# Performance work log

Measured on AMD Instinct MI355X. Metric: run time of the kernel, lower is better.

Reference implementation:

```python
import jax, jax.numpy as jnp
import numpy as np

D_MODEL = 2048
D_FFN = 8192
RANK = 16
MOD_SCALE = 0.1
EPS = 1e-6


def setup_inputs() -> dict:
    key = jax.random.key(0)
    ks = jax.random.split(key, 8)
    B, S = 2, 2048
    init_scale = 0.01
    return {
        'hidden_states': jax.random.normal(ks[0], (B, S, D_MODEL), jnp.float32),
        'attn_output': jax.random.normal(ks[1], (B, S, D_MODEL), jnp.float32),
        'A': jax.random.normal(ks[2], (D_MODEL, RANK), jnp.float32) * (init_scale / np.sqrt(D_MODEL)),
        'Bmat': jax.random.normal(ks[3], (RANK, D_FFN), jnp.float32) * (init_scale / np.sqrt(RANK)),
        'W_in': jax.random.normal(ks[4], (D_FFN, D_MODEL), jnp.float32) * 0.02,  # gate_proj.weight
        'W_up': jax.random.normal(ks[5], (D_FFN, D_MODEL), jnp.float32) * 0.02,  # up_proj.weight
        'W_down': jax.random.normal(ks[6], (D_MODEL, D_FFN), jnp.float32) * 0.02,  # down_proj.weight
        'gamma': jnp.ones((D_MODEL,), jnp.float32),  # post_attention_layernorm (RMSNorm) weight
    }


def _rmsnorm(x, gamma):
    var = jnp.mean(x * x, axis=-1, keepdims=True)
    return x * jax.lax.rsqrt(var + EPS) * gamma


def reference(hidden_states, attn_output, A, Bmat, W_in, W_up, W_down, gamma):
    residual = hidden_states
    # Neuro-plastic modulation: [B,S,r]
    modulation = MOD_SCALE * jnp.tanh(jnp.einsum('bsd,dr->bsr', attn_output, A))
    # NPT applies post-attn norm to the residual (not residual+attn)
    h = _rmsnorm(residual, gamma)  # [B,S,d_model]
    # Fused per-token weight delta: delta_w^T @ h == B^T ((A^T h) * mod)
    hA = jnp.einsum('bsd,dr->bsr', h, A)  # [B,S,r]
    delta_out = jnp.einsum('bsr,rf->bsf', hA * modulation, Bmat)  # [B,S,d_ffn]
    gate = jax.nn.silu(jnp.einsum('bsd,fd->bsf', h, W_in) + delta_out)
    up = jnp.einsum('bsd,fd->bsf', h, W_up)
    out = jnp.einsum('bsf,df->bsd', gate * up, W_down)
    return residual + out
```

## Files before the change

### kernel.cpp

```cpp
#include <hip/hip_runtime.h>
#include <cstdint>
#include <cstddef>

#define D_MODEL 2048
#define D_FFN   8192
#define RANK    16
#define EPS     1e-6f
#define MOD_SCALE 0.1f

typedef float    f32x4 __attribute__((ext_vector_type(4)));
typedef _Float16 half8 __attribute__((ext_vector_type(8)));

__device__ __forceinline__ void async_load16(const void* g, void* l) {
  __builtin_amdgcn_global_load_lds(
      (const __attribute__((address_space(1))) uint32_t*)g,
      (__attribute__((address_space(3))) uint32_t*)l,
      16, 0, 0);
}

__device__ __forceinline__ void stage_round(const _Float16* __restrict__ g,
                                            size_t stride, _Float16* l, int tid) {
  const int row = tid >> 3;
  const int cs  = (tid & 7) ^ (row & 7);
  async_load16(g + (size_t)row * stride + (size_t)cs * 8, l + tid * 8);
}

__device__ __forceinline__ half8 frag64(const _Float16* base, int row, int ck) {
  return *(const half8*)&base[row * 64 + ((ck ^ (row & 7)) * 8)];
}

#define BAR()   __builtin_amdgcn_s_barrier()
#define PRIO1() __builtin_amdgcn_s_setprio(1)
#define PRIO0() __builtin_amdgcn_s_setprio(0)
#define VMW(n)  asm volatile("s_waitcnt vmcnt(" #n ")" ::: "memory")

__global__ __launch_bounds__(256) void convert3_f32_f16(
    const float* __restrict__ s0, const float* __restrict__ s1,
    const float* __restrict__ s2,
    _Float16* __restrict__ d0, _Float16* __restrict__ d1,
    _Float16* __restrict__ d2)
{
  const int w = blockIdx.x >> 13;
  const float*   s = (w == 0) ? s0 : (w == 1) ? s1 : s2;
  _Float16*      d = (w == 0) ? d0 : (w == 1) ? d1 : d2;
  size_t i = ((size_t)(blockIdx.x & 8191) * 256 + threadIdx.x) * 8;
  f32x4 a = *(const f32x4*)(s + i);
  f32x4 b = *(const f32x4*)(s + i + 4);
  half8 h;
  #pragma unroll
  for (int j = 0; j < 4; ++j) { h[j] = (_Float16)a[j]; h[4+j] = (_Float16)b[j]; }
  *(half8*)(d + i) = h;
}

__global__ __launch_bounds__(256) void convert_f32_f16(
    const float* __restrict__ s, _Float16* __restrict__ d)
{
  size_t i = ((size_t)blockIdx.x * 256 + threadIdx.x) * 8;
  f32x4 a = *(const f32x4*)(s + i);
  f32x4 b = *(const f32x4*)(s + i + 4);
  half8 h;
  #pragma unroll
  for (int j = 0; j < 4; ++j) { h[j] = (_Float16)a[j]; h[4+j] = (_Float16)b[j]; }
  *(half8*)(d + i) = h;
}

__global__ __launch_bounds__(256) void prep_kernel(
    const float* __restrict__ hs, const float* __restrict__ attn,
    const float* __restrict__ Amat, const float* __restrict__ gamma,
    _Float16* __restrict__ h16, float* __restrict__ cmat)
{
  const int token = blockIdx.x;
  const int tid   = threadIdx.x;
  const int lane  = tid & 63;
  const int wv    = tid >> 6;
  const size_t tb = (size_t)token * D_MODEL;
  const int base  = tid * 8;

  f32x4 x0 = *(const f32x4*)(hs + tb + base);
  f32x4 x1 = *(const f32x4*)(hs + tb + base + 4);
  f32x4 a0 = *(const f32x4*)(attn + tb + base);
  f32x4 a1 = *(const f32x4*)(attn + tb + base + 4);

  float ss = 0.f;
  #pragma unroll
  for (int j = 0; j < 4; ++j) ss += x0[j]*x0[j] + x1[j]*x1[j];
  #pragma unroll
  for (int off = 32; off > 0; off >>= 1) ss += __shfl_xor(ss, off, 64);

  __shared__ float red[4];
  __shared__ float redp[4][RANK];
  __shared__ float redh[4][RANK];
  if (lane == 0) red[wv] = ss;
  __syncthreads();
  const float tot = red[0] + red[1] + red[2] + red[3];
  const float rms = rsqrtf(tot * (1.0f / D_MODEL) + EPS);

  f32x4 g0 = *(const f32x4*)(gamma + base);
  f32x4 g1 = *(const f32x4*)(gamma + base + 4);
  float hv[8], av[8];
  #pragma unroll
  for (int j = 0; j < 4; ++j) {
    hv[j]   = x0[j] * rms * g0[j];
    hv[4+j] = x1[j] * rms * g1[j];
    av[j]   = a0[j];
    av[4+j] = a1[j];
  }
  half8 hh;
  #pragma unroll
  for (int j = 0; j < 8; ++j) hh[j] = (_Float16)hv[j];
  *(half8*)(h16 + tb + base) = hh;

  float pa[RANK], ph[RANK];
  #pragma unroll
  for (int r = 0; r < RANK; ++r) { pa[r] = 0.f; ph[r] = 0.f; }
  #pragma unroll
  for (int e = 0; e < 8; ++e) {
    const f32x4* Ar = (const f32x4*)(Amat + (size_t)(base + e) * RANK);
    #pragma unroll
    for (int q = 0; q < 4; ++q) {
      f32x4 ar = Ar[q];
      #pragma unroll
      for (int j = 0; j < 4; ++j) {
        pa[q*4+j] += av[e] * ar[j];
        ph[q*4+j] += hv[e] * ar[j];
      }
    }
  }
  #pragma unroll
  for (int r = 0; r < RANK; ++r) {
    #pragma unroll
    for (int off = 32; off > 0; off >>= 1) {
      pa[r] += __shfl_xor(pa[r], off, 64);
      ph[r] += __shfl_xor(ph[r], off, 64);
    }
  }
  if (lane == 0) {
    #pragma unroll
    for (int r = 0; r < RANK; ++r) { redp[wv][r] = pa[r]; redh[wv][r] = ph[r]; }
  }
  __syncthreads();
  if (tid < RANK) {
    float sp = redp[0][tid] + redp[1][tid] + redp[2][tid] + redp[3][tid];
    float sh = redh[0][tid] + redh[1][tid] + redh[2][tid] + redh[3][tid];
    cmat[(size_t)token * RANK + tid] = sh * (MOD_SCALE * tanhf(sp));
  }
}

#define BGOFF 16384
#define BUOFF 24576

__global__ __launch_bounds__(512, 2) void gemm_gateup(
    const _Float16* __restrict__ h16,
    const _Float16* __restrict__ Wg16, const _Float16* __restrict__ Wu16,
    const float* __restrict__ cmat, const float* __restrict__ Bmat,
    _Float16* __restrict__ tmat)
{
  __shared__ __align__(16) _Float16 lds[2][32768];

  const int tid  = threadIdx.x;
  const int lane = tid & 63;
  const int wv   = tid >> 6;
  const int lr   = lane & 15;
  const int quad = lane >> 4;
  const int qb   = (wv >> 2) * 2;
  const int e    = wv & 3;
  const int wm   = (wv >> 2) * 128;

  const int lin = blockIdx.x;
  const int swz = (lin & 7) * 128 + (lin >> 3);
  const int gm0 = (swz & 15) * 256;
  const int gn0 = (swz >> 4) * 128;

  constexpr int NT = D_MODEL / 64;

  f32x4 accG[8][2], accU[8][2];
  #pragma unroll
  for (int i = 0; i < 8; ++i)
    #pragma unroll
    for (int j = 0; j < 2; ++j) {
      f32x4 z = {0.f, 0.f, 0.f, 0.f};
      accG[i][j] = z; accU[i][j] = z;
    }

#define STA(b,q,t)  stage_round(h16  + (size_t)(gm0 + (q)*64) * D_MODEL + (size_t)(t)*64, D_MODEL, &lds[b][(q)*4096], tid)
#define STBG(b,p,t) stage_round(Wg16 + (size_t)(gn0 + (p)*64) * D_MODEL + (size_t)(t)*64, D_MODEL, &lds[b][BGOFF + (p)*4096], tid)
#define STBU(b,p,t) stage_round(Wu16 + (size_t)(gn0 + (p)*64) * D_MODEL + (size_t)(t)*64, D_MODEL, &lds[b][BUOFF + (p)*4096], tid)

  STA(0,0,0);  STA(0,2,0);
  STBG(0,0,0); STBG(0,1,0);
  STBU(0,0,0); STBU(0,1,0);
  STA(0,1,0);  STA(0,3,0);
  STA(1,0,1);  STA(1,2,1);
  STBG(1,0,1); STBG(1,1,1);
  VMW(8); BAR();

  half8 af[4][2], bg[2][2], bu[2][2];

  for (int t = 0; t < NT; ++t) {
    const int cur = t & 1, nxt = cur ^ 1;
    const _Float16* A   = &lds[cur][0];
    const _Float16* Bgp = &lds[cur][BGOFF + e * 2048];
    const _Float16* Bup = &lds[cur][BUOFF + e * 2048];
    const bool s1 = (t + 1 < NT);
    const bool s2 = (t + 2 < NT);
    const bool deep = (t + 3 < NT);

    #pragma unroll
    for (int im = 0; im < 4; ++im)
      #pragma unroll
      for (int kk = 0; kk < 2; ++kk)
        af[im][kk] = frag64(A + (qb + 0) * 4096, im*16 + lr, kk*4 + quad);
    #pragma unroll
    for (int inn = 0; inn < 2; ++inn)
      #pragma unroll
      for (int kk = 0; kk < 2; ++kk)
        bg[inn][kk] = frag64(Bgp, inn*16 + lr, kk*4 + quad);
    if (s1) { STBU(nxt, 0, t+1); STBU(nxt, 1, t+1); }
    BAR();
    PRIO1();
    #pragma unroll
    for (int im = 0; im < 4; ++im)
      #pragma unroll
      for (int inn = 0; inn < 2; ++inn)
        #pragma unroll
        for (int kk = 0; kk < 2; ++kk)
          accG[im][inn] = __builtin_amdgcn_mfma_f32_16x16x32_f16(af[im][kk], bg[inn][kk], accG[im][inn], 0, 0, 0);
    PRIO0();
    if (deep) { VMW(8); } else { VMW(0); }
    BAR();

    #pragma unroll
    for (int inn = 0; inn < 2; ++inn)
      #pragma unroll
      for (int kk = 0; kk < 2; ++kk)
        bu[inn][kk] = frag64(Bup, inn*16 + lr, kk*4 + quad);
    if (s1) { STA(nxt, 1, t+1); STA(nxt, 3, t+1); }
    BAR();
    PRIO1();
    #pragma unroll
    for (int im = 0; im < 4; ++im)
      #pragma unroll
      for (int inn = 0; inn < 2; ++inn)
        #pragma unroll
        for (int kk = 0; kk < 2; ++kk)
          accU[im][inn] = __builtin_amdgcn_mfma_f32_16x16x32_f16(af[im][kk], bu[inn][kk], accU[im][inn], 0, 0, 0);
    PRIO0();
    if (deep) { VMW(8); } else { VMW(0); }
    BAR();

    #pragma unroll
    for (int im = 0; im < 4; ++im)
      #pragma unroll
      for (int kk = 0; kk < 2; ++kk)
        af[im][kk] = frag64(A + (qb + 1) * 4096, im*16 + lr, kk*4 + quad);
    if (s2) { STA(cur, 0, t+2); STA(cur, 2, t+2); }
    BAR();
    PRIO1();
    #pragma unroll
    for (int im = 0; im < 4; ++im)
      #pragma unroll
      for (int inn = 0; inn < 2; ++inn)
        #pragma unroll
        for (int kk = 0; kk < 2; ++kk)
          accG[4+im][inn] = __builtin_amdgcn_mfma_f32_16x16x32_f16(af[im][kk], bg[inn][kk], accG[4+im][inn], 0, 0, 0);
    PRIO0();
    BAR();

    if (s2) { STBG(cur, 0, t+2); STBG(cur, 1, t+2); }
    BAR();
    PRIO1();
    #pragma unroll
    for (int im = 0; im < 4; ++im)
      #pragma unroll
      for (int inn = 0; inn < 2; ++inn)
        #pragma unroll
        for (int kk = 0; kk < 2; ++kk)
          accU[4+im][inn] = __builtin_amdgcn_mfma_f32_16x16x32_f16(af[im][kk], bu[inn][kk], accU[4+im][inn], 0, 0, 0);
    PRIO0();
    if (deep) { VMW(8); } else { VMW(0); }
    BAR();
  }

  __syncthreads();
  _Float16* l0 = &lds[0][0];
  for (int i = tid; i < 8192; i += 512) {
    int m = i >> 5, k = i & 31;
    l0[i] = (k < RANK) ? (_Float16)cmat[(size_t)(gm0 + m) * RANK + k] : (_Float16)0.f;
  }
  for (int i = tid; i < 4096; i += 512) {
    int f = i >> 5, k = i & 31;
    l0[8192 + i] = (k < RANK) ? (_Float16)Bmat[(size_t)k * D_FFN + gn0 + f] : (_Float16)0.f;
  }
  __syncthreads();
  #pragma unroll
  for (int ai = 0; ai < 8; ++ai) {
    half8 cf = *(const half8*)&l0[(wm + ai*16 + lr) * 32 + quad * 8];
    #pragma unroll
    for (int inn = 0; inn < 2; ++inn) {
      half8 bd = *(const half8*)&l0[8192 + (e*32 + inn*16 + lr) * 32 + quad * 8];
      accG[ai][inn] = __builtin_amdgcn_mfma_f32_16x16x32_f16(cf, bd, accG[ai][inn], 0, 0, 0);
    }
  }

  #pragma unroll
  for (int ai = 0; ai < 8; ++ai)
    #pragma unroll
    for (int inn = 0; inn < 2; ++inn) {
      const int grow = gm0 + wm + ai*16 + quad*4;
      const int gcol = gn0 + e*32 + inn*16 + lr;
      #pragma unroll
      for (int r = 0; r < 4; ++r) {
        float g = accG[ai][inn][r];
        float u = accU[ai][inn][r];
        float s = g / (1.0f + __expf(-g));
        tmat[(size_t)(grow + r) * D_FFN + gcol] = (_Float16)(s * u);
      }
    }
#undef STA
#undef STBG
#undef STBU
}

__global__ __launch_bounds__(512, 2) void gemm_down(
    const _Float16* __restrict__ tmat, const _Float16* __restrict__ Wd16,
    const float* __restrict__ hs, float* __restrict__ out)
{
  __shared__ __align__(16) _Float16 lds[3][24576];

  const int tid  = threadIdx.x;
  const int lane = tid & 63;
  const int wv   = tid >> 6;
  const int lr   = lane & 15;
  const int quad = lane >> 4;
  const int qb   = (wv >> 2) * 2;
  const int e    = wv & 3;
  const int wm   = (wv >> 2) * 128;

  const int lin = blockIdx.x;
  const int swz = (lin & 7) * 32 + (lin >> 3);
  const int gm0 = (swz & 15) * 256;
  const int gn0 = (swz >> 4) * 128;

  constexpr int NT = D_FFN / 64;

  f32x4 acc[8][2];
  #pragma unroll
  for (int i = 0; i < 8; ++i)
    #pragma unroll
    for (int j = 0; j < 2; ++j) {
      f32x4 z = {0.f, 0.f, 0.f, 0.f};
      acc[i][j] = z;
    }

#define DSTA(b,q,t) stage_round(tmat + (size_t)(gm0 + (q)*64) * D_FFN + (size_t)(t)*64, D_FFN, &lds[b][(q)*4096], tid)
#define DSTB(b,p,t) stage_round(Wd16 + (size_t)(gn0 + (p)*64) * D_FFN + (size_t)(t)*64, D_FFN, &lds[b][16384 + (p)*4096], tid)

  DSTA(0,0,0); DSTA(0,1,0); DSTA(0,2,0); DSTA(0,3,0); DSTB(0,0,0); DSTB(0,1,0);
  DSTA(1,0,1); DSTA(1,1,1); DSTA(1,2,1); DSTA(1,3,1); DSTB(1,0,1); DSTB(1,1,1);
  VMW(6); BAR();

  half8 af[4][2], bf[2][2];
  int cur = 0;

  for (int t = 0; t < NT; ++t) {
    const _Float16* A = &lds[cur][0];
    const _Float16* B = &lds[cur][16384 + e * 2048];
    int nx2 = cur + 2; if (nx2 >= 3) nx2 -= 3;
    const bool s2 = (t + 2 < NT);
    const bool deep = (t + 3 < NT);

    #pragma unroll
    for (int im = 0; im < 4; ++im)
      #pragma unroll
      for (int kk = 0; kk < 2; ++kk)
        af[im][kk] = frag64(A + (qb + 0) * 4096, im*16 + lr, kk*4 + quad);
    #pragma unroll
    for (int inn = 0; inn < 2; ++inn)
      #pragma unroll
      for (int kk = 0; kk < 2; ++kk)
        bf[inn][kk] = frag64(B, inn*16 + lr, kk*4 + quad);
    if (s2) { DSTA(nx2, 0, t+2); DSTA(nx2, 2, t+2); DSTB(nx2, 0, t+2); }
    BAR();
    PRIO1();
    #pragma unroll
    for (int im = 0; im < 4; ++im)
      #pragma unroll
      for (int inn = 0; inn < 2; ++inn)
        #pragma unroll
        for (int kk = 0; kk < 2; ++kk)
          acc[im][inn] = __builtin_amdgcn_mfma_f32_16x16x32_f16(af[im][kk], bf[inn][kk], acc[im][inn], 0, 0, 0);
    PRIO0();
    BAR();

    #pragma unroll
    for (int im = 0; im < 4; ++im)
      #pragma unroll
      for (int kk = 0; kk < 2; ++kk)
        af[im][kk] = frag64(A + (qb + 1) * 4096, im*16 + lr, kk*4 + quad);
    if (s2) { DSTA(nx2, 1, t+2); DSTA(nx2, 3, t+2); DSTB(nx2, 1, t+2); }
    BAR();
    PRIO1();
    #pragma unroll
    for (int im = 0; im < 4; ++im)
      #pragma unroll
      for (int inn = 0; inn < 2; ++inn)
        #pragma unroll
        for (int kk = 0; kk < 2; ++kk)
          acc[4+im][inn] = __builtin_amdgcn_mfma_f32_16x16x32_f16(af[im][kk], bf[inn][kk], acc[4+im][inn], 0, 0, 0);
    PRIO0();
    if (deep) { VMW(6); } else { VMW(0); }
    BAR();

    cur += 1; if (cur >= 3) cur -= 3;
  }

  #pragma unroll
  for (int ai = 0; ai < 8; ++ai)
    #pragma unroll
    for (int inn = 0; inn < 2; ++inn) {
      const int grow = gm0 + wm + ai*16 + quad*4;
      const int gcol = gn0 + e*32 + inn*16 + lr;
      #pragma unroll
      for (int r = 0; r < 4; ++r) {
        size_t o = (size_t)(grow + r) * D_MODEL + gcol;
        out[o] = hs[o] + acc[ai][inn][r];
      }
    }
#undef DSTA
#undef DSTB
}

extern "C" void kernel_launch(void* const* d_in, const int* in_sizes, int n_in,
                              void* d_out, int out_size, void* d_ws, size_t ws_size,
                              hipStream_t stream) {
  const float* hs    = (const float*)d_in[0];
  const float* attn  = (const float*)d_in[1];
  const float* Amat  = (const float*)d_in[2];
  const float* Bmat  = (const float*)d_in[3];
  const float* Wg    = (const float*)d_in[4];
  const float* Wu    = (const float*)d_in[5];
  const float* Wd    = (const float*)d_in[6];
  const float* gamma = (const float*)d_in[7];
  float* out = (float*)d_out;

  const int M = in_sizes[0] / D_MODEL;
  const size_t WD = (size_t)D_FFN * D_MODEL;

  char* ws = (char*)d_ws;
  _Float16* h16  = (_Float16*)ws;
  float*    cmat = (float*)(ws + (size_t)M * D_MODEL * 2);
  _Float16* tmat = (_Float16*)(ws + (size_t)M * D_MODEL * 2 + (size_t)M * RANK * 4);
  _Float16* wbuf = tmat + (size_t)M * D_FFN;
  _Float16* Wg16 = wbuf;
  _Float16* Wu16 = wbuf + WD;

  const size_t base_bytes = (size_t)M * D_MODEL * 2 + (size_t)M * RANK * 4
                          + (size_t)M * D_FFN * 2 + 2 * WD * 2;
  const bool sep_wd = (ws_size >= base_bytes + WD * 2);
  _Float16* Wd16 = sep_wd ? (wbuf + 2 * WD) : wbuf;

  const int convBlocks = (int)(WD / (256 * 8));

  prep_kernel<<<M, 256, 0, stream>>>(hs, attn, Amat, gamma, h16, cmat);
  if (sep_wd) {
    convert3_f32_f16<<<3 * convBlocks, 256, 0, stream>>>(Wg, Wu, Wd, Wg16, Wu16, Wd16);
    gemm_gateup<<<dim3((D_FFN / 128) * (M / 256)), 512, 0, stream>>>(h16, Wg16, Wu16, cmat, Bmat, tmat);
  } else {
    convert_f32_f16<<<convBlocks, 256, 0, stream>>>(Wg, Wg16);
    convert_f32_f16<<<convBlocks, 256, 0, stream>>>(Wu, Wu16);
    gemm_gateup<<<dim3((D_FFN / 128) * (M / 256)), 512, 0, stream>>>(h16, Wg16, Wu16, cmat, Bmat, tmat);
    convert_f32_f16<<<convBlocks, 256, 0, stream>>>(Wd, Wd16);
  }
  gemm_down<<<dim3((D_MODEL / 128) * (M / 256)), 512, 0, stream>>>(tmat, Wd16, hs, out);
}
```

Baseline: 745.1 us.

## Simplify GEMM pipelines to whole-tile staging with one barrier per iteration and XCD-aware tile mapping

Both GEMMs drop the finely interleaved per-quarter staging with many barriers. gate/up now issues all loads for the next K tile at the top of each iteration and does a full vmcnt(0) wait plus one barrier at the end. down keeps a three-buffer, two-ahead prefetch with a single barrier per iteration. Block-to-tile mapping is changed so that each XCD shares A rows (gate/up) or B columns (down), aiming at better L2 reuse. The cost is that gate/up now has only one tile of prefetch distance and a full wait each iteration, which can expose memory latency.

```diff
diff --git a/kernel.cpp b/kernel.cpp
--- a/kernel.cpp
+++ b/kernel.cpp
@@ -29,10 +29,10 @@
   return *(const half8*)&base[row * 64 + ((ck ^ (row & 7)) * 8)];
 }
 
-#define BAR()   __builtin_amdgcn_s_barrier()
 #define PRIO1() __builtin_amdgcn_s_setprio(1)
 #define PRIO0() __builtin_amdgcn_s_setprio(0)
 #define VMW(n)  asm volatile("s_waitcnt vmcnt(" #n ")" ::: "memory")
+#define BARM()  asm volatile("s_barrier" ::: "memory")
 
 __global__ __launch_bounds__(256) void convert3_f32_f16(
     const float* __restrict__ s0, const float* __restrict__ s1,
@@ -166,10 +166,11 @@
   const int e    = wv & 3;
   const int wm   = (wv >> 2) * 128;
 
-  const int lin = blockIdx.x;
-  const int swz = (lin & 7) * 128 + (lin >> 3);
-  const int gm0 = (swz & 15) * 256;
-  const int gn0 = (swz >> 4) * 128;
+  const int lin  = blockIdx.x;
+  const int xcd  = lin & 7;
+  const int r    = lin >> 3;
+  const int gm0  = (xcd * 2 + (r & 1)) * 256;
+  const int gn0  = (r >> 1) * 128;
 
   constexpr int NT = D_MODEL / 64;
 
@@ -185,100 +186,66 @@
 #define STA(b,q,t)  stage_round(h16  + (size_t)(gm0 + (q)*64) * D_MODEL + (size_t)(t)*64, D_MODEL, &lds[b][(q)*4096], tid)
 #define STBG(b,p,t) stage_round(Wg16 + (size_t)(gn0 + (p)*64) * D_MODEL + (size_t)(t)*64, D_MODEL, &lds[b][BGOFF + (p)*4096], tid)
 #define STBU(b,p,t) stage_round(Wu16 + (size_t)(gn0 + (p)*64) * D_MODEL + (size_t)(t)*64, D_MODEL, &lds[b][BUOFF + (p)*4096], tid)
-
-  STA(0,0,0);  STA(0,2,0);
-  STBG(0,0,0); STBG(0,1,0);
-  STBU(0,0,0); STBU(0,1,0);
-  STA(0,1,0);  STA(0,3,0);
-  STA(1,0,1);  STA(1,2,1);
-  STBG(1,0,1); STBG(1,1,1);
-  VMW(8); BAR();
-
-  half8 af[4][2], bg[2][2], bu[2][2];
+#define STAGE_ALL(b,t) do { STA(b,0,t); STA(b,1,t); STA(b,2,t); STA(b,3,t); \
+                            STBG(b,0,t); STBG(b,1,t); STBU(b,0,t); STBU(b,1,t); } while (0)
+
+  STAGE_ALL(0, 0);
+  VMW(0); BARM();
 
   for (int t = 0; t < NT; ++t) {
     const int cur = t & 1, nxt = cur ^ 1;
     const _Float16* A   = &lds[cur][0];
     const _Float16* Bgp = &lds[cur][BGOFF + e * 2048];
     const _Float16* Bup = &lds[cur][BUOFF + e * 2048];
-    const bool s1 = (t + 1 < NT);
-    const bool s2 = (t + 2 < NT);
-    const bool deep = (t + 3 < NT);
-
+
+    if (t + 1 < NT) STAGE_ALL(nxt, t + 1);
+
+    half8 bg[2][2], bu[2][2], af[4][2];
+    #pragma unroll
+    for (int inn = 0; inn < 2; ++inn)
+      #pragma unroll
+      for (int kk = 0; kk < 2; ++kk) {
+        bg[inn][kk] = frag64(Bgp, inn*16 + lr, kk*4 + quad);
+        bu[inn][kk] = frag64(Bup, inn*16 + lr, kk*4 + quad);
+      }
     #pragma unroll
     for (int im = 0; im < 4; ++im)
       #pragma unroll
       for (int kk = 0; kk < 2; ++kk)
         af[im][kk] = frag64(A + (qb + 0) * 4096, im*16 + lr, kk*4 + quad);
-    #pragma unroll
-    for (int inn = 0; inn < 2; ++inn)
-      #pragma unroll
-      for (int kk = 0; kk < 2; ++kk)
-        bg[inn][kk] = frag64(Bgp, inn*16 + lr, kk*4 + quad);
-    if (s1) { STBU(nxt, 0, t+1); STBU(nxt, 1, t+1); }
-    BAR();
+
     PRIO1();
     #pragma unroll
     for (int im = 0; im < 4; ++im)
       #pragma unroll
       for (int inn = 0; inn < 2; ++inn)
         #pragma unroll
-        for (int kk = 0; kk < 2; ++kk)
+        for (int kk = 0; kk < 2; ++kk) {
           accG[im][inn] = __builtin_amdgcn_mfma_f32_16x16x32_f16(af[im][kk], bg[inn][kk], accG[im][inn], 0, 0, 0);
+          accU[im][inn] = __builtin_amdgcn_mfma_f32_16x16x32_f16(af[im][kk], bu[inn][kk], accU[im][inn], 0, 0, 0);
+        }
     PRIO0();
-    if (deep) { VMW(8); } else { VMW(0); }
-    BAR();
-
-    #pragma unroll
-    for (int inn = 0; inn < 2; ++inn)
+
+    half8 ao[4][2];
+    #pragma unroll
+    for (int im = 0; im < 4; ++im)
       #pragma unroll
       for (int kk = 0; kk < 2; ++kk)
-        bu[inn][kk] = frag64(Bup, inn*16 + lr, kk*4 + quad);
-    if (s1) { STA(nxt, 1, t+1); STA(nxt, 3, t+1); }
-    BAR();
+        ao[im][kk] = frag64(A + (qb + 1) * 4096, im*16 + lr, kk*4 + quad);
+
     PRIO1();
     #pragma unroll
     for (int im = 0; im < 4; ++im)
       #pragma unroll
       for (int inn = 0; inn < 2; ++inn)
         #pragma unroll
-        for (int kk = 0; kk < 2; ++kk)
-          accU[im][inn] = __builtin_amdgcn_mfma_f32_16x16x32_f16(af[im][kk], bu[inn][kk], accU[im][inn], 0, 0, 0);
+        for (int kk = 0; kk < 2; ++kk) {
+          accG[4+im][inn] = __builtin_amdgcn_mfma_f32_16x16x32_f16(ao[im][kk], bg[inn][kk], accG[4+im][inn], 0, 0, 0);
+          accU[4+im][inn] = __builtin_amdgcn_mfma_f32_16x16x32_f16(ao[im][kk], bu[inn][kk], accU[4+im][inn], 0, 0, 0);
+        }
     PRIO0();
-    if (deep) { VMW(8); } else { VMW(0); }
-    BAR();
-
-    #pragma unroll
-    for (int im = 0; im < 4; ++im)
-      #pragma unroll
-      for (int kk = 0; kk < 2; ++kk)
-        af[im][kk] = frag64(A + (qb + 1) * 4096, im*16 + lr, kk*4 + quad);
-    if (s2) { STA(cur, 0, t+2); STA(cur, 2, t+2); }
-    BAR();
-    PRIO1();
-    #pragma unroll
-    for (int im = 0; im < 4; ++im)
-      #pragma unroll
-      for (int inn = 0; inn < 2; ++inn)
-        #pragma unroll
-        for (int kk = 0; kk < 2; ++kk)
-          accG[4+im][inn] = __builtin_amdgcn_mfma_f32_16x16x32_f16(af[im][kk], bg[inn][kk], accG[4+im][inn], 0, 0, 0);
-    PRIO0();
-    BAR();
-
-    if (s2) { STBG(cur, 0, t+2); STBG(cur, 1, t+2); }
-    BAR();
-    PRIO1();
-    #pragma unroll
-    for (int im = 0; im < 4; ++im)
-      #pragma unroll
-      for (int inn = 0; inn < 2; ++inn)
-        #pragma unroll
-        for (int kk = 0; kk < 2; ++kk)
-          accU[4+im][inn] = __builtin_amdgcn_mfma_f32_16x16x32_f16(af[im][kk], bu[inn][kk], accU[4+im][inn], 0, 0, 0);
-    PRIO0();
-    if (deep) { VMW(8); } else { VMW(0); }
-    BAR();
+
+    VMW(0); BARM();
   }
 
   __syncthreads();
@@ -309,16 +276,17 @@
       const int grow = gm0 + wm + ai*16 + quad*4;
       const int gcol = gn0 + e*32 + inn*16 + lr;
       #pragma unroll
-      for (int r = 0; r < 4; ++r) {
-        float g = accG[ai][inn][r];
-        float u = accU[ai][inn][r];
+      for (int rr = 0; rr < 4; ++rr) {
+        float g = accG[ai][inn][rr];
+        float u = accU[ai][inn][rr];
         float s = g / (1.0f + __expf(-g));
-        tmat[(size_t)(grow + r) * D_FFN + gcol] = (_Float16)(s * u);
+        tmat[(size_t)(grow + rr) * D_FFN + gcol] = (_Float16)(s * u);
       }
     }
 #undef STA
 #undef STBG
 #undef STBU
+#undef STAGE_ALL
 }
 
 __global__ __launch_bounds__(512, 2) void gemm_down(
@@ -336,10 +304,11 @@
   const int e    = wv & 3;
   const int wm   = (wv >> 2) * 128;
 
-  const int lin = blockIdx.x;
-  const int swz = (lin & 7) * 32 + (lin >> 3);
-  const int gm0 = (swz & 15) * 256;
-  const int gn0 = (swz >> 4) * 128;
+  const int lin  = blockIdx.x;
+  const int xcd  = lin & 7;
+  const int r    = lin >> 3;
+  const int gn0  = (xcd * 2 + (r & 1)) * 128;
+  const int gm0  = (r >> 1) * 256;
 
   constexpr int NT = D_FFN / 64;
 
@@ -354,33 +323,33 @@
 
 #define DSTA(b,q,t) stage_round(tmat + (size_t)(gm0 + (q)*64) * D_FFN + (size_t)(t)*64, D_FFN, &lds[b][(q)*4096], tid)
 #define DSTB(b,p,t) stage_round(Wd16 + (size_t)(gn0 + (p)*64) * D_FFN + (size_t)(t)*64, D_FFN, &lds[b][16384 + (p)*4096], tid)
-
-  DSTA(0,0,0); DSTA(0,1,0); DSTA(0,2,0); DSTA(0,3,0); DSTB(0,0,0); DSTB(0,1,0);
-  DSTA(1,0,1); DSTA(1,1,1); DSTA(1,2,1); DSTA(1,3,1); DSTB(1,0,1); DSTB(1,1,1);
-  VMW(6); BAR();
-
-  half8 af[4][2], bf[2][2];
+#define DSTAGE_ALL(b,t) do { DSTA(b,0,t); DSTA(b,1,t); DSTA(b,2,t); DSTA(b,3,t); \
+                             DSTB(b,0,t); DSTB(b,1,t); } while (0)
+
+  DSTAGE_ALL(0, 0);
+  DSTAGE_ALL(1, 1);
+  VMW(6); BARM();
+
   int cur = 0;
-
   for (int t = 0; t < NT; ++t) {
     const _Float16* A = &lds[cur][0];
     const _Float16* B = &lds[cur][16384 + e * 2048];
     int nx2 = cur + 2; if (nx2 >= 3) nx2 -= 3;
-    const bool s2 = (t + 2 < NT);
-    const bool deep = (t + 3 < NT);
-
+
+    if (t + 2 < NT) DSTAGE_ALL(nx2, t + 2);
+
+    half8 bf[2][2], af[4][2];
+    #pragma unroll
+    for (int inn = 0; inn < 2; ++inn)
+      #pragma unroll
+      for (int kk = 0; kk < 2; ++kk)
+        bf[inn][kk] = frag64(B, inn*16 + lr, kk*4 + quad);
     #pragma unroll
     for (int im = 0; im < 4; ++im)
       #pragma unroll
       for (int kk = 0; kk < 2; ++kk)
         af[im][kk] = frag64(A + (qb + 0) * 4096, im*16 + lr, kk*4 + quad);
-    #pragma unroll
-    for (int inn = 0; inn < 2; ++inn)
-      #pragma unroll
-      for (int kk = 0; kk < 2; ++kk)
-        bf[inn][kk] = frag64(B, inn*16 + lr, kk*4 + quad);
-    if (s2) { DSTA(nx2, 0, t+2); DSTA(nx2, 2, t+2); DSTB(nx2, 0, t+2); }
-    BAR();
+
     PRIO1();
     #pragma unroll
     for (int im = 0; im < 4; ++im)
@@ -390,15 +359,14 @@
         for (int kk = 0; kk < 2; ++kk)
           acc[im][inn] = __builtin_amdgcn_mfma_f32_16x16x32_f16(af[im][kk], bf[inn][kk], acc[im][inn], 0, 0, 0);
     PRIO0();
-    BAR();
-
+
+    half8 ao[4][2];
     #pragma unroll
     for (int im = 0; im < 4; ++im)
       #pragma unroll
       for (int kk = 0; kk < 2; ++kk)
-        af[im][kk] = frag64(A + (qb + 1) * 4096, im*16 + lr, kk*4 + quad);
-    if (s2) { DSTA(nx2, 1, t+2); DSTA(nx2, 3, t+2); DSTB(nx2, 1, t+2); }
-    BAR();
+        ao[im][kk] = frag64(A + (qb + 1) * 4096, im*16 + lr, kk*4 + quad);
+
     PRIO1();
     #pragma unroll
     for (int im = 0; im < 4; ++im)
@@ -406,10 +374,11 @@
       for (int inn = 0; inn < 2; ++inn)
         #pragma unroll
         for (int kk = 0; kk < 2; ++kk)
-          acc[4+im][inn] = __builtin_amdgcn_mfma_f32_16x16x32_f16(af[im][kk], bf[inn][kk], acc[4+im][inn], 0, 0, 0);
+          acc[4+im][inn] = __builtin_amdgcn_mfma_f32_16x16x32_f16(ao[im][kk], bf[inn][kk], acc[4+im][inn], 0, 0, 0);
     PRIO0();
-    if (deep) { VMW(6); } else { VMW(0); }
-    BAR();
+
+    if (t + 2 < NT) { VMW(6); } else { VMW(0); }
+    BARM();
 
     cur += 1; if (cur >= 3) cur -= 3;
   }
@@ -421,13 +390,14 @@
       const int grow = gm0 + wm + ai*16 + quad*4;
       const int gcol = gn0 + e*32 + inn*16 + lr;
       #pragma unroll
-      for (int r = 0; r < 4; ++r) {
-        size_t o = (size_t)(grow + r) * D_MODEL + gcol;
-        out[o] = hs[o] + acc[ai][inn][r];
+      for (int rr = 0; rr < 4; ++rr) {
+        size_t o = (size_t)(grow + rr) * D_MODEL + gcol;
+        out[o] = hs[o] + acc[ai][inn][rr];
       }
     }
 #undef DSTA
 #undef DSTB
+#undef DSTAGE_ALL
 }
 
 extern "C" void kernel_launch(void* const* d_in, const int* in_sizes, int n_in,
```

Measured after the change: 734.7 us. Within noise of the previous version (-1.4%).
